# Kernel optimization log

Hardware: AMD Instinct MI355X
Metric: run time of the kernel (lower is better)

The kernel has to match this reference:

```python
import jax, jax.numpy as jnp
import numpy as np

B, N, F_IN = 8, 2048, 16
E, H = 64, 4
D = E // H
HID, A = 128, 4
QUEUE_IDX = np.array([0, 1, 2, 3, 6, 7, 8, 9, 10, 11, 12, 13])


def setup_inputs() -> dict:
    key = jax.random.key(0)
    ks = iter(jax.random.split(key, 64))
    def g(*s, scale=0.05):
        return jax.random.normal(next(ks), s, jnp.float32) * scale
    inp = {}
    inp['node_features'] = jax.random.normal(next(ks), (B, N, F_IN), jnp.float32) * 10.0
    inp['adjacency'] = jax.random.randint(next(ks), (B, N, N), 0, 2).astype(jnp.float32)
    for i, fin in enumerate([F_IN, E]):
        inp[f'l{i}_wq'] = g(fin, E)
        inp[f'l{i}_wk'] = g(fin, E)
        inp[f'l{i}_wv'] = g(fin, E)
        inp[f'l{i}_in_w'] = g(E, 3 * E)
        inp[f'l{i}_in_b'] = jnp.zeros(3 * E, jnp.float32)
        inp[f'l{i}_mha_ow'] = g(E, E)
        inp[f'l{i}_mha_ob'] = jnp.zeros(E, jnp.float32)
        inp[f'l{i}_op_w'] = g(E, E)
        inp[f'l{i}_op_b'] = jnp.zeros(E, jnp.float32)
    inp['head_w1'] = g(E, HID)
    inp['head_b1'] = jnp.zeros(HID, jnp.float32)
    inp['head_w2'] = g(HID, HID)
    inp['head_b2'] = jnp.zeros(HID, jnp.float32)
    inp['head_w3'] = g(HID, A, scale=0.001)
    inp['head_b3'] = jnp.zeros(A, jnp.float32)
    return inp


def _gat_layer(x, mask, wq, wk, wv, in_w, in_b, mow, mob, opw, opb):
    # x: [B,N,Fin], mask: [B,N,N] bool (True = blocked)
    b, n, _ = x.shape
    q = x @ wq  # layer's own Q/K/V projections (bias-free)
    k = x @ wk
    v = x @ wv
    # nn.MultiheadAttention's internal in_proj (with bias)
    Q = q @ in_w[:, :E] + in_b[:E]
    K = k @ in_w[:, E:2 * E] + in_b[E:2 * E]
    V = v @ in_w[:, 2 * E:] + in_b[2 * E:]
    Qh = Q.reshape(b, n, H, D)
    Kh = K.reshape(b, n, H, D)
    Vh = V.reshape(b, n, H, D)
    s = jnp.einsum('bqhd,bkhd->bhqk', Qh, Kh) / jnp.sqrt(jnp.float32(D))
    s = jnp.where(mask[:, None, :, :], -jnp.inf, s)
    a = jax.nn.softmax(s, axis=-1)  # diagonal always unmasked -> no all-inf rows
    o = jnp.einsum('bhqk,bkhd->bqhd', a, Vh).reshape(b, n, E)
    o = o @ mow + mob  # MHA out_proj
    return o @ opw + opb  # layer out_proj


def reference(node_features, adjacency,
              l0_wq, l0_wk, l0_wv, l0_in_w, l0_in_b, l0_mha_ow, l0_mha_ob, l0_op_w, l0_op_b,
              l1_wq, l1_wk, l1_wv, l1_in_w, l1_in_b, l1_mha_ow, l1_mha_ob, l1_op_w, l1_op_b,
              head_w1, head_b1, head_w2, head_b2, head_w3, head_b3):
    f = node_features.shape[-1]
    scale = jnp.ones(f, node_features.dtype).at[QUEUE_IDX].set(1.0 / 50.0).at[5].set(1.0 / 300.0)
    x = node_features * scale
    n = adjacency.shape[-1]
    mask = (adjacency + jnp.eye(n, dtype=adjacency.dtype)) == 0
    x = jax.nn.relu(_gat_layer(x, mask, l0_wq, l0_wk, l0_wv, l0_in_w, l0_in_b, l0_mha_ow, l0_mha_ob, l0_op_w, l0_op_b))
    x = jax.nn.relu(_gat_layer(x, mask, l1_wq, l1_wk, l1_wv, l1_in_w, l1_in_b, l1_mha_ow, l1_mha_ob, l1_op_w, l1_op_b))
    h = jax.nn.relu(x @ head_w1 + head_b1)
    h = jax.nn.relu(h @ head_w2 + head_b2)
    return h @ head_w3 + head_b3  # [B, N, n_actions]
```

## Files before the change

### kernel.cpp

```cpp
#include <hip/hip_runtime.h>

#define BB 8
#define NN 2048
#define FIN0 16
#define EE 64
#define HH 4
#define DD 16
#define HIDN 128
#define AA 4

__global__ __launch_bounds__(256) void k_mask(const float* __restrict__ adj, unsigned long long* __restrict__ mbT) {
    const int ITER = 32;
    for (int it = 0; it < ITER; it++) {
        long long idx = ((long long)blockIdx.x * ITER + it) * 256 + threadIdx.x;
        int k = (int)(idx & (NN - 1));
        int r = (int)((idx >> 11) & (NN - 1));
        int b = (int)(idx >> 22);
        float a = adj[idx];
        bool blocked = (a == 0.0f) && (k != r);
        unsigned long long m = __ballot(blocked);
        if ((threadIdx.x & 63) == 0) mbT[((long long)b * 32 + (k >> 6)) * NN + r] = m;
    }
}

#define QSCALE 0.36067376022224085f
__device__ __forceinline__ float sfeat(int f) {
    return (f == 4 || f == 14 || f == 15) ? 1.0f : ((f == 5) ? (1.0f / 300.0f) : 0.02f);
}
__global__ __launch_bounds__(256) void k_wcomb(
        const float* __restrict__ wq0, const float* __restrict__ wk0, const float* __restrict__ wv0,
        const float* __restrict__ inw0, const float* __restrict__ inb0,
        const float* __restrict__ mow0, const float* __restrict__ mob0,
        const float* __restrict__ opw0, const float* __restrict__ opb0,
        const float* __restrict__ wq1, const float* __restrict__ wk1, const float* __restrict__ wv1,
        const float* __restrict__ inw1, const float* __restrict__ inb1,
        const float* __restrict__ mow1, const float* __restrict__ mob1,
        const float* __restrict__ opw1, const float* __restrict__ opb1,
        float* __restrict__ CW0, float* __restrict__ WO0, float* __restrict__ bO0, float* __restrict__ bQ0,
        float* __restrict__ CW1, float* __restrict__ WO1, float* __restrict__ bO1, float* __restrict__ bQ1) {
    int ly = blockIdx.y;
    int fin = ly ? EE : FIN0;
    const float* wq = ly ? wq1 : wq0; const float* wk = ly ? wk1 : wk0; const float* wv = ly ? wv1 : wv0;
    const float* inw = ly ? inw1 : inw0; const float* inb = ly ? inb1 : inb0;
    const float* mow = ly ? mow1 : mow0; const float* mob = ly ? mob1 : mob0;
    const float* opw = ly ? opw1 : opw0; const float* opb = ly ? opb1 : opb0;
    float* CW = ly ? CW1 : CW0; float* WO = ly ? WO1 : WO0;
    float* bO = ly ? bO1 : bO0; float* bQ = ly ? bQ1 : bQ0;

    int t = blockIdx.x * 256 + threadIdx.x;
    int t1 = fin * 192;
    int t2 = t1 + 4096;
    int t3 = t2 + 64;
    int t4 = t3 + 192;
    if (t < t1) {
        int f = t / 192, j = t % 192;
        const float* w = (j < 64) ? wq : ((j < 128) ? wk : wv);
        float acc = 0.f;
        for (int kk = 0; kk < 64; kk++) acc += w[f * 64 + kk] * inw[kk * 192 + j];
        if (j < 64) acc *= QSCALE;
        if (ly == 0) acc *= sfeat(f);
        CW[t] = acc;
    } else if (t < t2) {
        int u = t - t1; int i = u >> 6, j = u & 63;
        float acc = 0.f;
        for (int kk = 0; kk < 64; kk++) acc += mow[i * 64 + kk] * opw[kk * 64 + j];
        WO[u] = acc;
    } else if (t < t3) {
        int j = t - t2;
        float acc = opb[j];
        for (int kk = 0; kk < 64; kk++) acc += mob[kk] * opw[kk * 64 + j];
        bO[j] = acc;
    } else if (t < t4) {
        int j = t - t3;
        bQ[j] = inb[j] * ((j < 64) ? QSCALE : 1.0f);
    }
}

template <int FINP>
__global__ __launch_bounds__(256) void k_qkv(const float* __restrict__ X, const float* __restrict__ CW,
                                             const float* __restrict__ bQ,
                                             float* __restrict__ Q, float* __restrict__ K, float* __restrict__ V) {
    int lane = threadIdx.x & 63;
    int quarter = threadIdx.x >> 6;
    int row = blockIdx.x * 64 + lane;
    int b = row >> 11, n = row & (NN - 1);
    float xr[FINP];
    const float4* xp = (const float4*)(X + (long long)row * FINP);
#pragma unroll
    for (int i = 0; i < FINP / 4; i++) {
        float4 v = xp[i];
        xr[4 * i] = v.x; xr[4 * i + 1] = v.y; xr[4 * i + 2] = v.z; xr[4 * i + 3] = v.w;
    }
    for (int jq = 0; jq < 12; jq++) {
        int j = quarter * 48 + jq * 4;
        float4 acc = *(const float4*)(bQ + j);
#pragma unroll
        for (int f = 0; f < FINP; f++) {
            float4 w = *(const float4*)(CW + f * 192 + j);
            acc.x = fmaf(xr[f], w.x, acc.x);
            acc.y = fmaf(xr[f], w.y, acc.y);
            acc.z = fmaf(xr[f], w.z, acc.z);
            acc.w = fmaf(xr[f], w.w, acc.w);
        }
        int which = j >> 6, c = j & 63, h = c >> 4, d = c & 15;
        float* dst = (which == 0) ? Q : ((which == 1) ? K : V);
        *(float4*)(dst + (((long long)(b * HH + h) * NN + n) * DD + d)) = acc;
    }
}

__global__ __launch_bounds__(512, 2) void k_attn(const float* __restrict__ Q, const float* __restrict__ K,
                                                 const float* __restrict__ V,
                                                 const unsigned long long* __restrict__ mbT,
                                                 float* __restrict__ O) {
    __shared__ float smem[8 * 4 * 64 * 17];
    int lane = threadIdx.x & 63;
    int w = threadIdx.x >> 6;
    int qb = blockIdx.x, h = blockIdx.y, b = blockIdx.z;
    int qbase = qb * 256;

    const float* Qbh = Q + (long long)(b * HH + h) * NN * DD;
    const float* Kb  = K + (long long)(b * HH + h) * NN * DD;
    const float* Vb  = V + (long long)(b * HH + h) * NN * DD;
    const unsigned long long* mrow = mbT + (long long)b * 32 * NN;

    float4 qf[4][4];
#pragma unroll
    for (int rq = 0; rq < 4; rq++) {
        const float4* qp = (const float4*)(Qbh + (long long)(qbase + rq * 64 + lane) * DD);
#pragma unroll
        for (int j = 0; j < 4; j++) qf[rq][j] = qp[j];
    }
    float4 oacc[4][4];
#pragma unroll
    for (int rq = 0; rq < 4; rq++)
#pragma unroll
        for (int j = 0; j < 4; j++) oacc[rq][j] = make_float4(0.f, 0.f, 0.f, 0.f);
    float lsum[4] = {0.f, 0.f, 0.f, 0.f};

    const float4* kp = (const float4*)(Kb + (long long)(w * 256) * DD);
    const float4* vp = (const float4*)(Vb + (long long)(w * 256) * DD);

    float4 kc[4], vc[4];
#pragma unroll
    for (int i = 0; i < 4; i++) { kc[i] = kp[i]; vc[i] = vp[i]; }
    unsigned long long mwpre[4];
#pragma unroll
    for (int rq = 0; rq < 4; rq++) mwpre[rq] = mrow[(long long)(w * 4) * NN + qbase + rq * 64 + lane];

    for (int c = 0; c < 4; c++) {
        unsigned long long mw[4];
#pragma unroll
        for (int rq = 0; rq < 4; rq++) mw[rq] = mwpre[rq];
        {
            int kblkn = w * 4 + c + 1;
#pragma unroll
            for (int rq = 0; rq < 4; rq++) mwpre[rq] = mrow[(long long)kblkn * NN + qbase + rq * 64 + lane];
        }
#pragma unroll 4
        for (int kk = 0; kk < 64; kk++) {
            int idx = c * 64 + kk;
            float4 kn[4], vn[4];
#pragma unroll
            for (int i = 0; i < 4; i++) { kn[i] = kp[(idx + 1) * 4 + i]; vn[i] = vp[(idx + 1) * 4 + i]; }
            float4 k0 = kc[0], k1 = kc[1], k2 = kc[2], k3 = kc[3];
            float e[4];
#pragma unroll
            for (int rq = 0; rq < 4; rq++) {
                float4 a0 = qf[rq][0], a1 = qf[rq][1], a2 = qf[rq][2], a3 = qf[rq][3];
                float sA = a0.x * k0.x;
                sA = fmaf(a0.y, k0.y, sA); sA = fmaf(a0.z, k0.z, sA); sA = fmaf(a0.w, k0.w, sA);
                sA = fmaf(a1.x, k1.x, sA); sA = fmaf(a1.y, k1.y, sA); sA = fmaf(a1.z, k1.z, sA); sA = fmaf(a1.w, k1.w, sA);
                float sB = a2.x * k2.x;
                sB = fmaf(a2.y, k2.y, sB); sB = fmaf(a2.z, k2.z, sB); sB = fmaf(a2.w, k2.w, sB);
                sB = fmaf(a3.x, k3.x, sB); sB = fmaf(a3.y, k3.y, sB); sB = fmaf(a3.z, k3.z, sB); sB = fmaf(a3.w, k3.w, sB);
                float ee = __builtin_amdgcn_exp2f(sA + sB);
                e[rq] = ((mw[rq] >> kk) & 1ULL) ? 0.f : ee;
                lsum[rq] += e[rq];
            }
            float4 v0 = vc[0], v1 = vc[1], v2 = vc[2], v3 = vc[3];
#pragma unroll
            for (int rq = 0; rq < 4; rq++) {
                float ew = e[rq];
                oacc[rq][0].x = fmaf(ew, v0.x, oacc[rq][0].x); oacc[rq][0].y = fmaf(ew, v0.y, oacc[rq][0].y);
                oacc[rq][0].z = fmaf(ew, v0.z, oacc[rq][0].z); oacc[rq][0].w = fmaf(ew, v0.w, oacc[rq][0].w);
                oacc[rq][1].x = fmaf(ew, v1.x, oacc[rq][1].x); oacc[rq][1].y = fmaf(ew, v1.y, oacc[rq][1].y);
                oacc[rq][1].z = fmaf(ew, v1.z, oacc[rq][1].z); oacc[rq][1].w = fmaf(ew, v1.w, oacc[rq][1].w);
                oacc[rq][2].x = fmaf(ew, v2.x, oacc[rq][2].x); oacc[rq][2].y = fmaf(ew, v2.y, oacc[rq][2].y);
                oacc[rq][2].z = fmaf(ew, v2.z, oacc[rq][2].z); oacc[rq][2].w = fmaf(ew, v2.w, oacc[rq][2].w);
                oacc[rq][3].x = fmaf(ew, v3.x, oacc[rq][3].x); oacc[rq][3].y = fmaf(ew, v3.y, oacc[rq][3].y);
                oacc[rq][3].z = fmaf(ew, v3.z, oacc[rq][3].z); oacc[rq][3].w = fmaf(ew, v3.w, oacc[rq][3].w);
            }
#pragma unroll
            for (int i = 0; i < 4; i++) { kc[i] = kn[i]; vc[i] = vn[i]; }
        }
    }
    __syncthreads();
#pragma unroll
    for (int rq = 0; rq < 4; rq++) {
        float* rp = smem + (((w * 4 + rq) * 64 + lane)) * 17;
#pragma unroll
        for (int j = 0; j < 4; j++) {
            rp[4 * j + 0] = oacc[rq][j].x; rp[4 * j + 1] = oacc[rq][j].y;
            rp[4 * j + 2] = oacc[rq][j].z; rp[4 * j + 3] = oacc[rq][j].w;
        }
        rp[16] = lsum[rq];
    }
    __syncthreads();
    if (w < 4) {
        int rq = w;
        float acc[DD]; float lt = 0.f;
#pragma unroll
        for (int d = 0; d < DD; d++) acc[d] = 0.f;
#pragma unroll
        for (int p = 0; p < 8; p++) {
            const float* pp = smem + (((p * 4 + rq) * 64 + lane)) * 17;
#pragma unroll
            for (int d = 0; d < DD; d++) acc[d] += pp[d];
            lt += pp[16];
        }
        float inv = 1.0f / lt;
        int q = qbase + rq * 64 + lane;
        float* op = O + (long long)(b * NN + q) * EE + h * DD;
        float4 r0 = {acc[0]*inv, acc[1]*inv, acc[2]*inv, acc[3]*inv};
        float4 r1 = {acc[4]*inv, acc[5]*inv, acc[6]*inv, acc[7]*inv};
        float4 r2 = {acc[8]*inv, acc[9]*inv, acc[10]*inv, acc[11]*inv};
        float4 r3 = {acc[12]*inv, acc[13]*inv, acc[14]*inv, acc[15]*inv};
        ((float4*)op)[0] = r0; ((float4*)op)[1] = r1; ((float4*)op)[2] = r2; ((float4*)op)[3] = r3;
    }
}

__global__ __launch_bounds__(256) void k_out(const float* __restrict__ X, const float* __restrict__ WO,
                                             const float* __restrict__ bO, float* __restrict__ Y) {
    int lane = threadIdx.x & 63, quarter = threadIdx.x >> 6;
    long long row = (long long)blockIdx.x * 64 + lane;
    float xr[64];
    const float4* xp = (const float4*)(X + row * 64);
#pragma unroll
    for (int i = 0; i < 16; i++) {
        float4 t = xp[i];
        xr[4 * i] = t.x; xr[4 * i + 1] = t.y; xr[4 * i + 2] = t.z; xr[4 * i + 3] = t.w;
    }
    for (int jq = 0; jq < 4; jq++) {
        int j = quarter * 16 + jq * 4;
        float4 acc = *(const float4*)(bO + j);
#pragma unroll
        for (int f = 0; f < 64; f++) {
            float4 w4 = *(const float4*)(WO + f * 64 + j);
            acc.x = fmaf(xr[f], w4.x, acc.x);
            acc.y = fmaf(xr[f], w4.y, acc.y);
            acc.z = fmaf(xr[f], w4.z, acc.z);
            acc.w = fmaf(xr[f], w4.w, acc.w);
        }
        acc.x = fmaxf(acc.x, 0.f); acc.y = fmaxf(acc.y, 0.f);
        acc.z = fmaxf(acc.z, 0.f); acc.w = fmaxf(acc.w, 0.f);
        *(float4*)(Y + row * 64 + j) = acc;
    }
}

__global__ __launch_bounds__(256) void k_outqkv(const float* __restrict__ O, const float* __restrict__ WO,
                                                const float* __restrict__ bO,
                                                const float* __restrict__ CW, const float* __restrict__ bQ,
                                                float* __restrict__ Q, float* __restrict__ K, float* __restrict__ V) {
    __shared__ float xs[64 * 68];
    int lane = threadIdx.x & 63, quarter = threadIdx.x >> 6;
    long long row = (long long)blockIdx.x * 64 + lane;
    int b = (int)(row >> 11), n = (int)(row & (NN - 1));
    {
        float xr[64];
        const float4* xp = (const float4*)(O + row * 64);
#pragma unroll
        for (int i = 0; i < 16; i++) {
            float4 t = xp[i];
            xr[4 * i] = t.x; xr[4 * i + 1] = t.y; xr[4 * i + 2] = t.z; xr[4 * i + 3] = t.w;
        }
        for (int jq = 0; jq < 4; jq++) {
            int j = quarter * 16 + jq * 4;
            float4 acc = *(const float4*)(bO + j);
#pragma unroll
            for (int f = 0; f < 64; f++) {
                float4 w4 = *(const float4*)(WO + f * 64 + j);
                acc.x = fmaf(xr[f], w4.x, acc.x);
                acc.y = fmaf(xr[f], w4.y, acc.y);
                acc.z = fmaf(xr[f], w4.z, acc.z);
                acc.w = fmaf(xr[f], w4.w, acc.w);
            }
            acc.x = fmaxf(acc.x, 0.f); acc.y = fmaxf(acc.y, 0.f);
            acc.z = fmaxf(acc.z, 0.f); acc.w = fmaxf(acc.w, 0.f);
            *(float4*)(xs + lane * 68 + j) = acc;
        }
    }
    __syncthreads();
    {
        float xr[64];
        const float4* xp = (const float4*)(xs + lane * 68);
#pragma unroll
        for (int i = 0; i < 16; i++) {
            float4 t = xp[i];
            xr[4 * i] = t.x; xr[4 * i + 1] = t.y; xr[4 * i + 2] = t.z; xr[4 * i + 3] = t.w;
        }
        for (int jq = 0; jq < 12; jq++) {
            int j = quarter * 48 + jq * 4;
            float4 acc = *(const float4*)(bQ + j);
#pragma unroll
            for (int f = 0; f < 64; f++) {
                float4 w4 = *(const float4*)(CW + f * 192 + j);
                acc.x = fmaf(xr[f], w4.x, acc.x);
                acc.y = fmaf(xr[f], w4.y, acc.y);
                acc.z = fmaf(xr[f], w4.z, acc.z);
                acc.w = fmaf(xr[f], w4.w, acc.w);
            }
            int which = j >> 6, c = j & 63, h = c >> 4, d = c & 15;
            float* dst = (which == 0) ? Q : ((which == 1) ? K : V);
            *(float4*)(dst + (((long long)(b * HH + h) * NN + n) * DD + d)) = acc;
        }
    }
}

__global__ __launch_bounds__(128) void k_head(const float* __restrict__ X,
                                              const float* __restrict__ w1, const float* __restrict__ b1,
                                              const float* __restrict__ w2, const float* __restrict__ b2,
                                              const float* __restrict__ w3, const float* __restrict__ b3,
                                              float* __restrict__ out) {
    __shared__ float Xs[16 * 64];
    __shared__ float H1[16 * 132];
    __shared__ float H2[16 * 132];
    int tid = threadIdx.x;
    long long row0 = (long long)blockIdx.x * 16;
    {
        const float4* src = (const float4*)(X + row0 * 64);
        float4* dst = (float4*)Xs;
        dst[tid] = src[tid];
        dst[tid + 128] = src[tid + 128];
    }
    __syncthreads();
    {
        float wr[64];
#pragma unroll
        for (int f = 0; f < 64; f++) wr[f] = w1[f * 128 + tid];
        float bb = b1[tid];
        for (int r = 0; r < 16; r++) {
            const float4* x4 = (const float4*)(Xs + r * 64);
            float a0 = bb, a1 = 0.f, a2 = 0.f, a3 = 0.f;
#pragma unroll
            for (int fq = 0; fq < 16; fq++) {
                float4 xv = x4[fq];
                a0 = fmaf(xv.x, wr[4 * fq], a0);
                a1 = fmaf(xv.y, wr[4 * fq + 1], a1);
                a2 = fmaf(xv.z, wr[4 * fq + 2], a2);
                a3 = fmaf(xv.w, wr[4 * fq + 3], a3);
            }
            H1[r * 132 + tid] = fmaxf((a0 + a1) + (a2 + a3), 0.f);
        }
    }
    __syncthreads();
    {
        float acc2[16];
        float bb2 = b2[tid];
#pragma unroll
        for (int r = 0; r < 16; r++) acc2[r] = bb2;
#pragma unroll
        for (int p = 0; p < 2; p++) {
            float wr2[64];
#pragma unroll
            for (int i = 0; i < 64; i++) wr2[i] = w2[(p * 64 + i) * 128 + tid];
            for (int r = 0; r < 16; r++) {
                const float4* h4 = (const float4*)(H1 + r * 132 + p * 64);
                float a0 = 0.f, a1 = 0.f, a2 = 0.f, a3 = 0.f;
#pragma unroll
                for (int fq = 0; fq < 16; fq++) {
                    float4 xv = h4[fq];
                    a0 = fmaf(xv.x, wr2[4 * fq], a0);
                    a1 = fmaf(xv.y, wr2[4 * fq + 1], a1);
                    a2 = fmaf(xv.z, wr2[4 * fq + 2], a2);
                    a3 = fmaf(xv.w, wr2[4 * fq + 3], a3);
                }
                acc2[r] += (a0 + a1) + (a2 + a3);
            }
        }
#pragma unroll
        for (int r = 0; r < 16; r++) H2[r * 132 + tid] = fmaxf(acc2[r], 0.f);
    }
    __syncthreads();
    if (tid < 64) {
        int r = tid >> 2, a = tid & 3;
        float acc = b3[a];
        for (int f = 0; f < 128; f++) acc = fmaf(H2[r * 132 + f], w3[f * 4 + a], acc);
        out[(row0 + r) * 4 + a] = acc;
    }
}

extern "C" void kernel_launch(void* const* d_in, const int* in_sizes, int n_in,
                              void* d_out, int out_size, void* d_ws, size_t ws_size,
                              hipStream_t stream) {
    const float* nf = (const float*)d_in[0];
    const float* adj = (const float*)d_in[1];
    const float* l0[9]; for (int i = 0; i < 9; i++) l0[i] = (const float*)d_in[2 + i];
    const float* l1[9]; for (int i = 0; i < 9; i++) l1[i] = (const float*)d_in[11 + i];
    const float* hw1 = (const float*)d_in[20]; const float* hb1 = (const float*)d_in[21];
    const float* hw2 = (const float*)d_in[22]; const float* hb2 = (const float*)d_in[23];
    const float* hw3 = (const float*)d_in[24]; const float* hb3 = (const float*)d_in[25];
    float* out = (float*)d_out;

    char* ws = (char*)d_ws;
    size_t off = 0;
    auto alloc = [&](size_t bytes) -> void* {
        void* p = ws + off;
        off = (off + bytes + 255) & ~(size_t)255;
        return p;
    };
    unsigned long long* mbT = (unsigned long long*)alloc((size_t)BB * NN * NN / 8);
    float* Q = (float*)alloc((size_t)BB * HH * NN * DD * 4);
    float* K = (float*)alloc((size_t)BB * HH * NN * DD * 4);
    float* V = (float*)alloc((size_t)BB * HH * NN * DD * 4);
    float* O = (float*)alloc((size_t)BB * NN * EE * 4);
    float* x2 = (float*)alloc((size_t)BB * NN * EE * 4);
    float* CW0 = (float*)alloc(16 * 192 * 4);
    float* CW1 = (float*)alloc(64 * 192 * 4);
    float* WO0 = (float*)alloc(64 * 64 * 4);
    float* WO1 = (float*)alloc(64 * 64 * 4);
    float* bO0 = (float*)alloc(64 * 4);
    float* bO1 = (float*)alloc(64 * 4);
    float* bQ0 = (float*)alloc(192 * 4);
    float* bQ1 = (float*)alloc(192 * 4);

    k_mask<<<4096, 256, 0, stream>>>(adj, mbT);
    k_wcomb<<<dim3(65, 2), 256, 0, stream>>>(
        l0[0], l0[1], l0[2], l0[3], l0[4], l0[5], l0[6], l0[7], l0[8],
        l1[0], l1[1], l1[2], l1[3], l1[4], l1[5], l1[6], l1[7], l1[8],
        CW0, WO0, bO0, bQ0, CW1, WO1, bO1, bQ1);

    k_qkv<16><<<BB * NN / 64, 256, 0, stream>>>(nf, CW0, bQ0, Q, K, V);
    k_attn<<<dim3(NN / 256, HH, BB), 512, 0, stream>>>(Q, K, V, mbT, O);
    k_outqkv<<<BB * NN / 64, 256, 0, stream>>>(O, WO0, bO0, CW1, bQ1, Q, K, V);
    k_attn<<<dim3(NN / 256, HH, BB), 512, 0, stream>>>(Q, K, V, mbT, O);
    k_out<<<BB * NN / 64, 256, 0, stream>>>(O, WO1, bO1, x2);
    k_head<<<BB * NN / 16, 128, 0, stream>>>(x2, hw1, hb1, hw2, hb2, hw3, hb3, out);
}
```

Baseline: 648.2 us.

## Retile attention to 128 queries per block with double-buffered K/V prefetch

The attention kernel now gives each block 128 queries and 256 threads. Each wave holds 2 query rows instead of 4 and walks 512 keys instead of 256. K/V rows are prefetched two steps ahead using alternating register buffers, and the mask words are loaded per chunk rather than software-prefetched. Halving per-thread query state cuts register pressure and doubles the block count, but each loaded K/V row is reused across fewer queries, so K/V traffic rises. The launch bound also changes to 1 block per SM.

```diff
diff --git a/kernel.cpp b/kernel.cpp
--- a/kernel.cpp
+++ b/kernel.cpp
@@ -108,96 +108,99 @@
     }
 }
 
-__global__ __launch_bounds__(512, 2) void k_attn(const float* __restrict__ Q, const float* __restrict__ K,
-                                                 const float* __restrict__ V,
-                                                 const unsigned long long* __restrict__ mbT,
-                                                 float* __restrict__ O) {
-    __shared__ float smem[8 * 4 * 64 * 17];
+__global__ __launch_bounds__(256, 1)
+void k_attn(const float* __restrict__ Q, const float* __restrict__ K,
+            const float* __restrict__ V,
+            const unsigned long long* __restrict__ mbT,
+            float* __restrict__ O) {
+    __shared__ float smem[4 * 2 * 64 * 17];
     int lane = threadIdx.x & 63;
     int w = threadIdx.x >> 6;
     int qb = blockIdx.x, h = blockIdx.y, b = blockIdx.z;
-    int qbase = qb * 256;
+    int qbase = qb * 128;
 
     const float* Qbh = Q + (long long)(b * HH + h) * NN * DD;
     const float* Kb  = K + (long long)(b * HH + h) * NN * DD;
     const float* Vb  = V + (long long)(b * HH + h) * NN * DD;
     const unsigned long long* mrow = mbT + (long long)b * 32 * NN;
 
-    float4 qf[4][4];
-#pragma unroll
-    for (int rq = 0; rq < 4; rq++) {
+    float4 qf[2][4];
+#pragma unroll
+    for (int rq = 0; rq < 2; rq++) {
         const float4* qp = (const float4*)(Qbh + (long long)(qbase + rq * 64 + lane) * DD);
 #pragma unroll
         for (int j = 0; j < 4; j++) qf[rq][j] = qp[j];
     }
-    float4 oacc[4][4];
-#pragma unroll
-    for (int rq = 0; rq < 4; rq++)
+    float4 oacc[2][4];
+#pragma unroll
+    for (int rq = 0; rq < 2; rq++)
 #pragma unroll
         for (int j = 0; j < 4; j++) oacc[rq][j] = make_float4(0.f, 0.f, 0.f, 0.f);
-    float lsum[4] = {0.f, 0.f, 0.f, 0.f};
-
-    const float4* kp = (const float4*)(Kb + (long long)(w * 256) * DD);
-    const float4* vp = (const float4*)(Vb + (long long)(w * 256) * DD);
-
-    float4 kc[4], vc[4];
-#pragma unroll
-    for (int i = 0; i < 4; i++) { kc[i] = kp[i]; vc[i] = vp[i]; }
-    unsigned long long mwpre[4];
-#pragma unroll
-    for (int rq = 0; rq < 4; rq++) mwpre[rq] = mrow[(long long)(w * 4) * NN + qbase + rq * 64 + lane];
-
-    for (int c = 0; c < 4; c++) {
-        unsigned long long mw[4];
-#pragma unroll
-        for (int rq = 0; rq < 4; rq++) mw[rq] = mwpre[rq];
-        {
-            int kblkn = w * 4 + c + 1;
-#pragma unroll
-            for (int rq = 0; rq < 4; rq++) mwpre[rq] = mrow[(long long)kblkn * NN + qbase + rq * 64 + lane];
-        }
+    float lsum[2] = {0.f, 0.f};
+
+    const float4* kp4 = (const float4*)(Kb + (long long)(w * 512) * DD);
+    const float4* vp4 = (const float4*)(Vb + (long long)(w * 512) * DD);
+
+    float4 kA[4], vA[4], kB[4], vB[4];
+#pragma unroll
+    for (int i = 0; i < 4; i++) { kA[i] = kp4[i]; vA[i] = vp4[i]; kB[i] = kp4[4 + i]; vB[i] = vp4[4 + i]; }
+
+    for (int c = 0; c < 8; c++) {
+        int kblk = w * 8 + c;
+        unsigned long long mw0 = mrow[(long long)kblk * NN + qbase + lane];
+        unsigned long long mw1 = mrow[(long long)kblk * NN + qbase + 64 + lane];
 #pragma unroll 4
-        for (int kk = 0; kk < 64; kk++) {
+        for (int kk = 0; kk < 64; kk += 2) {
             int idx = c * 64 + kk;
-            float4 kn[4], vn[4];
-#pragma unroll
-            for (int i = 0; i < 4; i++) { kn[i] = kp[(idx + 1) * 4 + i]; vn[i] = vp[(idx + 1) * 4 + i]; }
-            float4 k0 = kc[0], k1 = kc[1], k2 = kc[2], k3 = kc[3];
-            float e[4];
-#pragma unroll
-            for (int rq = 0; rq < 4; rq++) {
-                float4 a0 = qf[rq][0], a1 = qf[rq][1], a2 = qf[rq][2], a3 = qf[rq][3];
-                float sA = a0.x * k0.x;
-                sA = fmaf(a0.y, k0.y, sA); sA = fmaf(a0.z, k0.z, sA); sA = fmaf(a0.w, k0.w, sA);
-                sA = fmaf(a1.x, k1.x, sA); sA = fmaf(a1.y, k1.y, sA); sA = fmaf(a1.z, k1.z, sA); sA = fmaf(a1.w, k1.w, sA);
-                float sB = a2.x * k2.x;
-                sB = fmaf(a2.y, k2.y, sB); sB = fmaf(a2.z, k2.z, sB); sB = fmaf(a2.w, k2.w, sB);
-                sB = fmaf(a3.x, k3.x, sB); sB = fmaf(a3.y, k3.y, sB); sB = fmaf(a3.z, k3.z, sB); sB = fmaf(a3.w, k3.w, sB);
-                float ee = __builtin_amdgcn_exp2f(sA + sB);
-                e[rq] = ((mw[rq] >> kk) & 1ULL) ? 0.f : ee;
-                lsum[rq] += e[rq];
+#pragma unroll 2
+            for (int par = 0; par < 2; par++) {
+                float4 k0, k1, k2, k3, v0, v1, v2, v3;
+                if (par == 0) {
+                    k0 = kA[0]; k1 = kA[1]; k2 = kA[2]; k3 = kA[3];
+                    v0 = vA[0]; v1 = vA[1]; v2 = vA[2]; v3 = vA[3];
+#pragma unroll
+                    for (int i = 0; i < 4; i++) { kA[i] = kp4[(idx + 2) * 4 + i]; vA[i] = vp4[(idx + 2) * 4 + i]; }
+                } else {
+                    k0 = kB[0]; k1 = kB[1]; k2 = kB[2]; k3 = kB[3];
+                    v0 = vB[0]; v1 = vB[1]; v2 = vB[2]; v3 = vB[3];
+#pragma unroll
+                    for (int i = 0; i < 4; i++) { kB[i] = kp4[(idx + 3) * 4 + i]; vB[i] = vp4[(idx + 3) * 4 + i]; }
+                }
+                int bit = kk + par;
+                float e[2];
+#pragma unroll
+                for (int rq = 0; rq < 2; rq++) {
+                    float4 a0 = qf[rq][0], a1 = qf[rq][1], a2 = qf[rq][2], a3 = qf[rq][3];
+                    float sA = a0.x * k0.x;
+                    sA = fmaf(a0.y, k0.y, sA); sA = fmaf(a0.z, k0.z, sA); sA = fmaf(a0.w, k0.w, sA);
+                    sA = fmaf(a1.x, k1.x, sA); sA = fmaf(a1.y, k1.y, sA); sA = fmaf(a1.z, k1.z, sA); sA = fmaf(a1.w, k1.w, sA);
+                    float sB = a2.x * k2.x;
+                    sB = fmaf(a2.y, k2.y, sB); sB = fmaf(a2.z, k2.z, sB); sB = fmaf(a2.w, k2.w, sB);
+                    sB = fmaf(a3.x, k3.x, sB); sB = fmaf(a3.y, k3.y, sB); sB = fmaf(a3.z, k3.z, sB); sB = fmaf(a3.w, k3.w, sB);
+                    float ee = __builtin_amdgcn_exp2f(sA + sB);
+                    unsigned long long mwv = rq ? mw1 : mw0;
+                    e[rq] = ((mwv >> bit) & 1ULL) ? 0.f : ee;
+                    lsum[rq] += e[rq];
+                }
+#pragma unroll
+                for (int rq = 0; rq < 2; rq++) {
+                    float ew = e[rq];
+                    oacc[rq][0].x = fmaf(ew, v0.x, oacc[rq][0].x); oacc[rq][0].y = fmaf(ew, v0.y, oacc[rq][0].y);
+                    oacc[rq][0].z = fmaf(ew, v0.z, oacc[rq][0].z); oacc[rq][0].w = fmaf(ew, v0.w, oacc[rq][0].w);
+                    oacc[rq][1].x = fmaf(ew, v1.x, oacc[rq][1].x); oacc[rq][1].y = fmaf(ew, v1.y, oacc[rq][1].y);
+                    oacc[rq][1].z = fmaf(ew, v1.z, oacc[rq][1].z); oacc[rq][1].w = fmaf(ew, v1.w, oacc[rq][1].w);
+                    oacc[rq][2].x = fmaf(ew, v2.x, oacc[rq][2].x); oacc[rq][2].y = fmaf(ew, v2.y, oacc[rq][2].y);
+                    oacc[rq][2].z = fmaf(ew, v2.z, oacc[rq][2].z); oacc[rq][2].w = fmaf(ew, v2.w, oacc[rq][2].w);
+                    oacc[rq][3].x = fmaf(ew, v3.x, oacc[rq][3].x); oacc[rq][3].y = fmaf(ew, v3.y, oacc[rq][3].y);
+                    oacc[rq][3].z = fmaf(ew, v3.z, oacc[rq][3].z); oacc[rq][3].w = fmaf(ew, v3.w, oacc[rq][3].w);
+                }
             }
-            float4 v0 = vc[0], v1 = vc[1], v2 = vc[2], v3 = vc[3];
-#pragma unroll
-            for (int rq = 0; rq < 4; rq++) {
-                float ew = e[rq];
-                oacc[rq][0].x = fmaf(ew, v0.x, oacc[rq][0].x); oacc[rq][0].y = fmaf(ew, v0.y, oacc[rq][0].y);
-                oacc[rq][0].z = fmaf(ew, v0.z, oacc[rq][0].z); oacc[rq][0].w = fmaf(ew, v0.w, oacc[rq][0].w);
-                oacc[rq][1].x = fmaf(ew, v1.x, oacc[rq][1].x); oacc[rq][1].y = fmaf(ew, v1.y, oacc[rq][1].y);
-                oacc[rq][1].z = fmaf(ew, v1.z, oacc[rq][1].z); oacc[rq][1].w = fmaf(ew, v1.w, oacc[rq][1].w);
-                oacc[rq][2].x = fmaf(ew, v2.x, oacc[rq][2].x); oacc[rq][2].y = fmaf(ew, v2.y, oacc[rq][2].y);
-                oacc[rq][2].z = fmaf(ew, v2.z, oacc[rq][2].z); oacc[rq][2].w = fmaf(ew, v2.w, oacc[rq][2].w);
-                oacc[rq][3].x = fmaf(ew, v3.x, oacc[rq][3].x); oacc[rq][3].y = fmaf(ew, v3.y, oacc[rq][3].y);
-                oacc[rq][3].z = fmaf(ew, v3.z, oacc[rq][3].z); oacc[rq][3].w = fmaf(ew, v3.w, oacc[rq][3].w);
-            }
-#pragma unroll
-            for (int i = 0; i < 4; i++) { kc[i] = kn[i]; vc[i] = vn[i]; }
-        }
-    }
-    __syncthreads();
-#pragma unroll
-    for (int rq = 0; rq < 4; rq++) {
-        float* rp = smem + (((w * 4 + rq) * 64 + lane)) * 17;
+        }
+    }
+    __syncthreads();
+#pragma unroll
+    for (int rq = 0; rq < 2; rq++) {
+        float* rp = smem + (((w * 2 + rq) * 64 + lane)) * 17;
 #pragma unroll
         for (int j = 0; j < 4; j++) {
             rp[4 * j + 0] = oacc[rq][j].x; rp[4 * j + 1] = oacc[rq][j].y;
@@ -206,14 +209,14 @@
         rp[16] = lsum[rq];
     }
     __syncthreads();
-    if (w < 4) {
+    if (w < 2) {
         int rq = w;
         float acc[DD]; float lt = 0.f;
 #pragma unroll
         for (int d = 0; d < DD; d++) acc[d] = 0.f;
 #pragma unroll
-        for (int p = 0; p < 8; p++) {
-            const float* pp = smem + (((p * 4 + rq) * 64 + lane)) * 17;
+        for (int p = 0; p < 4; p++) {
+            const float* pp = smem + (((p * 2 + rq) * 64 + lane)) * 17;
 #pragma unroll
             for (int d = 0; d < DD; d++) acc[d] += pp[d];
             lt += pp[16];
@@ -430,9 +433,9 @@
         CW0, WO0, bO0, bQ0, CW1, WO1, bO1, bQ1);
 
     k_qkv<16><<<BB * NN / 64, 256, 0, stream>>>(nf, CW0, bQ0, Q, K, V);
-    k_attn<<<dim3(NN / 256, HH, BB), 512, 0, stream>>>(Q, K, V, mbT, O);
+    k_attn<<<dim3(NN / 128, HH, BB), 256, 0, stream>>>(Q, K, V, mbT, O);
     k_outqkv<<<BB * NN / 64, 256, 0, stream>>>(O, WO0, bO0, CW1, bQ1, Q, K, V);
-    k_attn<<<dim3(NN / 256, HH, BB), 512, 0, stream>>>(Q, K, V, mbT, O);
+    k_attn<<<dim3(NN / 128, HH, BB), 256, 0, stream>>>(Q, K, V, mbT, O);
     k_out<<<BB * NN / 64, 256, 0, stream>>>(O, WO1, bO1, x2);
     k_head<<<BB * NN / 16, 128, 0, stream>>>(x2, hw1, hb1, hw2, hb2, hw3, hb3, out);
 }
```

Result: slower. 848.9 us (+31.0%).
